# Kernel optimization log

Hardware: AMD Instinct MI355X
Metric: run time of the kernel (lower is better)

## Reference

```python
import jax, jax.numpy as jnp
import numpy as np

DIM = 768
NUM_HEADS = 12
HEAD_DIM = DIM // NUM_HEADS
SCALE = HEAD_DIM ** -0.5


def setup_inputs() -> dict:
    key = jax.random.key(0)
    ks = jax.random.split(key, 6)
    B, N, C = 4, 2048, DIM
    x = jax.random.normal(ks[0], (B, N, C), dtype=jnp.float32)
    qkv_weight = jax.random.normal(ks[1], (3 * C, C), dtype=jnp.float32) * (C ** -0.5)
    q_bias = jax.random.normal(ks[2], (C,), dtype=jnp.float32) * 0.02
    v_bias = jax.random.normal(ks[3], (C,), dtype=jnp.float32) * 0.02
    proj_weight = jax.random.normal(ks[4], (C, C), dtype=jnp.float32) * (C ** -0.5)
    proj_bias = jax.random.normal(ks[5], (C,), dtype=jnp.float32) * 0.02
    return {"x": x, "qkv_weight": qkv_weight, "q_bias": q_bias,
            "v_bias": v_bias, "proj_weight": proj_weight, "proj_bias": proj_bias}


def reference(x, qkv_weight, q_bias, v_bias, proj_weight, proj_bias):
    B, N, C = x.shape
    # bias = concat(q_bias, zeros_like(v_bias), v_bias)
    bias = jnp.concatenate([q_bias, jnp.zeros_like(v_bias), v_bias])
    qkv = x @ qkv_weight.T + bias                      # [B, N, 3C]
    qkv = qkv.reshape(B, N, 3, NUM_HEADS, HEAD_DIM)
    q, k, v = jnp.moveaxis(qkv, 2, 0)                  # each [B, N, H, hd]
    q = jnp.transpose(q, (0, 2, 1, 3)) * SCALE         # [B, H, N, hd]
    k = jnp.transpose(k, (0, 2, 1, 3))
    v = jnp.transpose(v, (0, 2, 1, 3))
    attn = jax.nn.softmax(jnp.einsum('bhqd,bhkd->bhqk', q, k), axis=-1)
    out = jnp.einsum('bhqk,bhkd->bhqd', attn, v)       # [B, H, N, hd]
    out = jnp.transpose(out, (0, 2, 1, 3)).reshape(B, N, C)
    return out @ proj_weight.T + proj_bias
```

## Files before the change

### kernel.cpp

```cpp
#include <hip/hip_runtime.h>
#include <cstdint>
#include <cstddef>

typedef _Float16 f16;
typedef _Float16 f16x8 __attribute__((ext_vector_type(8)));
typedef _Float16 f16x4 __attribute__((ext_vector_type(4)));
typedef __fp16 h16x2 __attribute__((ext_vector_type(2)));
typedef float f32x4 __attribute__((ext_vector_type(4)));
typedef float f32x16 __attribute__((ext_vector_type(16)));

#define DIM 768
#define NHEAD 12
#define HD 64
#define BATCH 4
#define SEQ 2048
#define MROWS (BATCH*SEQ)
#define C3 (3*DIM)
#define NBH (BATCH*NHEAD)

__device__ __forceinline__ f32x4 mfma32(f16x8 a, f16x8 b, f32x4 c) {
  return __builtin_amdgcn_mfma_f32_16x16x32_f16(a, b, c, 0, 0, 0);
}
__device__ __forceinline__ f32x16 mfma3232(f16x8 a, f16x8 b, f32x16 c) {
  return __builtin_amdgcn_mfma_f32_32x32x16_f16(a, b, c, 0, 0, 0);
}

__device__ __forceinline__ void gl2lds16(const void* g, void* l) {
  __builtin_amdgcn_global_load_lds(
      (const __attribute__((address_space(1))) void*)g,
      (__attribute__((address_space(3))) void*)l, 16, 0, 0);
}

__global__ __launch_bounds__(256) void k_convert(
    const float* __restrict__ x, const float* __restrict__ wqkv,
    const float* __restrict__ wproj,
    f16* __restrict__ xh, f16* __restrict__ wqh, f16* __restrict__ wph)
{
  const int NX = MROWS*DIM/4, NW = C3*DIM/4;
  int i = blockIdx.x * 256 + threadIdx.x;
  const float4* src; f16* dst; int idx;
  if (i < NX)         { src = (const float4*)x;     dst = xh;  idx = i; }
  else if (i < NX+NW) { src = (const float4*)wqkv;  dst = wqh; idx = i - NX; }
  else                { src = (const float4*)wproj; dst = wph; idx = i - NX - NW; }
  float4 v = src[idx];
  union { f16 h[4]; uint64_t u; } r;
  r.h[0] = (f16)v.x; r.h[1] = (f16)v.y; r.h[2] = (f16)v.z; r.h[3] = (f16)v.w;
  ((uint64_t*)dst)[idx] = r.u;
}

__device__ __forceinline__ void gemm_tile(
    const f16* __restrict__ A, const f16* __restrict__ B,
    int lda, int ldb, int K, int am0, int bn0,
    f16* smem, f32x4 acc[4][4])
{
  f16* sA0 = smem;         f16* sA1 = smem + 4096;
  f16* sB0 = smem + 8192;  f16* sB1 = smem + 12288;
  const int tid = threadIdx.x, wid = tid >> 6;
  const int lane = tid & 63, lane15 = lane & 15, quad = lane >> 4;
  const int wm = wid >> 1, wn = wid & 1;

  auto stage = [&](int k0, f16* sA, f16* sB) {
    #pragma unroll
    for (int i = 0; i < 2; i++) {
      int j = i*256 + tid;
      int row = j >> 2;
      int sc  = (j & 3) ^ ((row >> 1) & 3);
      gl2lds16(A + (size_t)(am0 + row)*lda + k0 + sc*8, sA + (i*256 + wid*64)*8);
      gl2lds16(B + (size_t)(bn0 + row)*ldb + k0 + sc*8, sB + (i*256 + wid*64)*8);
    }
  };

  const int NK = K >> 5;
  stage(0, sA0, sB0);
  for (int kk = 0; kk < NK; kk++) {
    f16* cA = (kk & 1) ? sA1 : sA0;
    f16* cB = (kk & 1) ? sB1 : sB0;
    __syncthreads();
    if (kk + 1 < NK)
      stage((kk + 1) << 5, (kk & 1) ? sA0 : sA1, (kk & 1) ? sB0 : sB1);
    f16x8 af[4], bf[4];
    #pragma unroll
    for (int t = 0; t < 4; t++) {
      int ra = wm*64 + t*16 + lane15;
      af[t] = *(const f16x8*)(cA + ra*32 + ((quad ^ ((ra >> 1) & 3)) << 3));
      int rb = wn*64 + t*16 + lane15;
      bf[t] = *(const f16x8*)(cB + rb*32 + ((quad ^ ((rb >> 1) & 3)) << 3));
    }
    #pragma unroll
    for (int mt = 0; mt < 4; mt++)
      #pragma unroll
      for (int nt = 0; nt < 4; nt++)
        acc[mt][nt] = mfma32(af[mt], bf[nt], acc[mt][nt]);
  }
}

__global__ __launch_bounds__(256, 4) void k_qkv(
    const f16* __restrict__ xh, const f16* __restrict__ wqh,
    const float* __restrict__ q_bias, const float* __restrict__ v_bias,
    f16* __restrict__ Qh, f16* __restrict__ Kh, f16* __restrict__ Vt)
{
  __shared__ f16 smem[16384];
  f32x4 acc[4][4];
  const f32x4 z4 = {0.f, 0.f, 0.f, 0.f};
  #pragma unroll
  for (int a = 0; a < 4; a++)
    #pragma unroll
    for (int b = 0; b < 4; b++) acc[a][b] = z4;

  const int tid = threadIdx.x, wid = tid >> 6, lane = tid & 63;
  const int lane15 = lane & 15, quad = lane >> 4;
  const int wm = wid >> 1, wn = wid & 1;
  const int cblk = blockIdx.x * 128;
  const int mblk = blockIdx.y * 128;
  const int bb = mblk >> 11, nbase = mblk & (SEQ - 1);
  const float QS = 0.125f * 1.4426950408889634f;

  if (cblk < 2*DIM) {
    gemm_tile(wqh, xh, DIM, DIM, DIM, cblk, mblk, smem, acc);
    const bool isQ = (cblk < DIM);
    #pragma unroll
    for (int mt = 0; mt < 4; mt++) {
      int c0 = cblk + wm*64 + mt*16 + quad*4;
      int cr = isQ ? c0 : (c0 - DIM);
      int h = cr >> 6, d0 = cr & 63;
      float4 qb4 = isQ ? *(const float4*)(q_bias + c0) : make_float4(0,0,0,0);
      f16* dst = isQ ? Qh : Kh;
      f16* base = dst + (((size_t)(bb*NHEAD + h)*SEQ + nbase) << 6) + d0;
      #pragma unroll
      for (int nt = 0; nt < 4; nt++) {
        int n = wn*64 + nt*16 + lane15;
        f32x4 v = acc[mt][nt];
        f16x4 hv;
        if (isQ) {
          hv[0] = (f16)((v[0] + qb4.x) * QS); hv[1] = (f16)((v[1] + qb4.y) * QS);
          hv[2] = (f16)((v[2] + qb4.z) * QS); hv[3] = (f16)((v[3] + qb4.w) * QS);
        } else {
          hv[0] = (f16)v[0]; hv[1] = (f16)v[1]; hv[2] = (f16)v[2]; hv[3] = (f16)v[3];
        }
        *(f16x4*)(base + ((size_t)n << 6)) = hv;
      }
    }
  } else {
    gemm_tile(xh, wqh, DIM, DIM, DIM, mblk, cblk, smem, acc);
    #pragma unroll
    for (int nt = 0; nt < 4; nt++) {
      int c = cblk + wn*64 + nt*16 + lane15;
      int c2 = c - 2*DIM;
      int h = c2 >> 6, d = c2 & 63;
      float b = v_bias[c2];
      f16* base = Vt + ((size_t)(bb*NHEAD + h)*HD + d)*SEQ + nbase;
      #pragma unroll
      for (int mt = 0; mt < 4; mt++) {
        int n0 = wm*64 + mt*16 + quad*4;
        f32x4 v = acc[mt][nt];
        f16x4 hv = {(f16)(v[0]+b), (f16)(v[1]+b), (f16)(v[2]+b), (f16)(v[3]+b)};
        *(f16x4*)(base + n0) = hv;
      }
    }
  }
}

#define KVT 128
#define NIT (SEQ/KVT)
__global__ __launch_bounds__(256, 3) void k_attn(
    const f16* __restrict__ Qh, const f16* __restrict__ Kh,
    const f16* __restrict__ Vt, f16* __restrict__ attnh)
{
  __shared__ f16 smem[2*8192 + 64*132];
  f16* sK0 = smem;
  f16* sK1 = smem + 8192;
  f16* sV  = smem + 16384;

  const int tid = threadIdx.x, wid = tid >> 6, lane = tid & 63;
  const int l31 = lane & 31, hi = lane >> 5;

  const int L = blockIdx.x;
  const int xcd = L & 7, kk = L >> 3;
  const int bh = xcd + 8*(kk >> 4);
  const int q0 = (kk & 15) * 128;
  const int qw = q0 + wid*32;

  const f16* Kbh = Kh + (size_t)bh*SEQ*HD;
  const f16* Vbh = Vt + (size_t)bh*HD*SEQ;

  f16x8 qf[4];
  #pragma unroll
  for (int ks = 0; ks < 4; ks++)
    qf[ks] = *(const f16x8*)(Qh + ((size_t)bh*SEQ + qw + l31)*HD + ks*16 + hi*8);

  const f32x16 z16 = {0.f,0.f,0.f,0.f, 0.f,0.f,0.f,0.f,
                      0.f,0.f,0.f,0.f, 0.f,0.f,0.f,0.f};
  f32x16 o0 = z16, o1 = z16, sacc = z16;
  f16x8 one8;
  #pragma unroll
  for (int j = 0; j < 8; j++) one8[j] = (f16)1.f;

  auto stageK = [&](int kv0, f16* sK) {
    #pragma unroll
    for (int i = 0; i < 4; i++) {
      int j = i*256 + tid;
      int row = j >> 3;
      int sc  = (j & 7) ^ (row & 7);
      gl2lds16(Kbh + (size_t)(kv0 + row)*HD + sc*8, sK + (i*256 + wid*64)*8);
    }
  };

  int koff[4];
  #pragma unroll
  for (int ks = 0; ks < 4; ks++)
    koff[ks] = l31*64 + (((2*ks + hi) ^ (l31 & 7)) << 3);

  const int vrow = tid >> 2, vcg = (tid & 3) * 32;
  const f16* vsrc = Vbh + (size_t)vrow*SEQ + vcg;

  stageK(0, sK0);
  f16x8 vreg[4];
  #pragma unroll
  for (int j = 0; j < 4; j++) vreg[j] = *(const f16x8*)(vsrc + j*8);

#define ASTEP(SCUR, SNXT, CC, HASNXT)                                         \
  do {                                                                        \
    const int vo = (CC)*32 + 4*hi;                                            \
    union { f16x4 q[2]; f16x8 v; } a00, a01, a10, a11;                        \
    a00.q[0] = *(const f16x4*)(sV + l31*132 + vo);                            \
    a00.q[1] = *(const f16x4*)(sV + l31*132 + vo + 8);                        \
    a01.q[0] = *(const f16x4*)(sV + l31*132 + vo + 16);                       \
    a01.q[1] = *(const f16x4*)(sV + l31*132 + vo + 24);                       \
    a10.q[0] = *(const f16x4*)(sV + (32 + l31)*132 + vo);                     \
    a10.q[1] = *(const f16x4*)(sV + (32 + l31)*132 + vo + 8);                 \
    a11.q[0] = *(const f16x4*)(sV + (32 + l31)*132 + vo + 16);                \
    a11.q[1] = *(const f16x4*)(sV + (32 + l31)*132 + vo + 24);                \
    unsigned hx[8];                                                           \
    _Pragma("unroll")                                                         \
    for (int r = 0; r < 8; r++) {                                             \
      union { h16x2 p2; unsigned u; } uu;                                     \
      uu.p2 = __builtin_amdgcn_cvt_pkrtz(                                     \
          __builtin_amdgcn_exp2f((SCUR)[2*r]),                                \
          __builtin_amdgcn_exp2f((SCUR)[2*r+1]));                             \
      hx[r] = uu.u;                                                           \
    }                                                                         \
    union { unsigned w[4]; f16x8 v; } b0u, b1u;                               \
    b0u.w[0]=hx[0]; b0u.w[1]=hx[1]; b0u.w[2]=hx[2]; b0u.w[3]=hx[3];           \
    b1u.w[0]=hx[4]; b1u.w[1]=hx[5]; b1u.w[2]=hx[6]; b1u.w[3]=hx[7];           \
    if (HASNXT) {                                                             \
      (SNXT) = z16;                                                           \
      __builtin_amdgcn_s_setprio(1);                                          \
      _Pragma("unroll")                                                       \
      for (int ks = 0; ks < 4; ks++) {                                        \
        f16x8 ka = *(const f16x8*)(cK + ((CC)+1)*2048 + koff[ks]);            \
        (SNXT) = mfma3232(ka, qf[ks], (SNXT));                                \
      }                                                                       \
      __builtin_amdgcn_s_setprio(0);                                          \
    }                                                                         \
    __builtin_amdgcn_s_setprio(1);                                            \
    sacc = mfma3232(one8, b0u.v, sacc);                                       \
    o0 = mfma3232(a00.v, b0u.v, o0);                                          \
    o1 = mfma3232(a10.v, b0u.v, o1);                                          \
    sacc = mfma3232(one8, b1u.v, sacc);                                       \
    o0 = mfma3232(a01.v, b1u.v, o0);                                          \
    o1 = mfma3232(a11.v, b1u.v, o1);                                          \
    __builtin_amdgcn_s_setprio(0);                                            \
  } while (0)

  for (int it = 0; it < NIT; it++) {
    f16* cK = (it & 1) ? sK1 : sK0;
    __syncthreads();
    #pragma unroll
    for (int j = 0; j < 4; j++) {
      union { f16x8 v; f16x4 h[2]; } u; u.v = vreg[j];
      *(f16x4*)(sV + vrow*132 + vcg + j*8)     = u.h[0];
      *(f16x4*)(sV + vrow*132 + vcg + j*8 + 4) = u.h[1];
    }
    __syncthreads();
    if (it + 1 < NIT) {
      stageK((it + 1)*KVT, (it & 1) ? sK0 : sK1);
      #pragma unroll
      for (int j = 0; j < 4; j++)
        vreg[j] = *(const f16x8*)(vsrc + (it + 1)*KVT + j*8);
    }

    f32x16 s0, s1;
    s0 = z16;
    __builtin_amdgcn_s_setprio(1);
    #pragma unroll
    for (int ks = 0; ks < 4; ks++) {
      f16x8 ka = *(const f16x8*)(cK + koff[ks]);
      s0 = mfma3232(ka, qf[ks], s0);
    }
    __builtin_amdgcn_s_setprio(0);
    ASTEP(s0, s1, 0, 1);
    ASTEP(s1, s0, 1, 1);
    ASTEP(s0, s1, 2, 1);
    ASTEP(s1, s0, 3, 0);
  }
#undef ASTEP

  const float inv = 1.f / sacc[0];

  __syncthreads();
  f16* tb = smem + wid * (32 * 72);
  #pragma unroll
  for (int g = 0; g < 4; g++) {
    f16x4 h0v = {(f16)(o0[4*g+0]*inv), (f16)(o0[4*g+1]*inv),
                 (f16)(o0[4*g+2]*inv), (f16)(o0[4*g+3]*inv)};
    *(f16x4*)(tb + l31*72 + g*8 + hi*4) = h0v;
    f16x4 h1v = {(f16)(o1[4*g+0]*inv), (f16)(o1[4*g+1]*inv),
                 (f16)(o1[4*g+2]*inv), (f16)(o1[4*g+3]*inv)};
    *(f16x4*)(tb + l31*72 + 32 + g*8 + hi*4) = h1v;
  }
  __syncthreads();
  const int b = bh / NHEAD, hh = bh % NHEAD;
  #pragma unroll
  for (int i = 0; i < 4; i++) {
    int row = i*8 + (lane >> 3);
    f16x8 rv = *(const f16x8*)(tb + row*72 + (lane & 7)*8);
    *(f16x8*)(attnh + ((size_t)b*SEQ + qw + row)*DIM + hh*HD + (lane & 7)*8) = rv;
  }
}

__global__ __launch_bounds__(256, 4) void k_proj(
    const f16* __restrict__ ah, const f16* __restrict__ wph,
    const float* __restrict__ pbias, float* __restrict__ out)
{
  __shared__ f16 smem[16384];
  f32x4 acc[4][4];
  const f32x4 z4 = {0.f, 0.f, 0.f, 0.f};
  #pragma unroll
  for (int a = 0; a < 4; a++)
    #pragma unroll
    for (int b = 0; b < 4; b++) acc[a][b] = z4;

  const int cblk = blockIdx.y * 128;
  const int mblk = blockIdx.x * 128;
  gemm_tile(wph, ah, DIM, DIM, DIM, cblk, mblk, smem, acc);

  const int tid = threadIdx.x, wid = tid >> 6, lane = tid & 63;
  const int lane15 = lane & 15, quad = lane >> 4;
  const int wm = wid >> 1, wn = wid & 1;
  #pragma unroll
  for (int mt = 0; mt < 4; mt++) {
    int c0 = cblk + wm*64 + mt*16 + quad*4;
    float4 b4 = *(const float4*)(pbias + c0);
    #pragma unroll
    for (int nt = 0; nt < 4; nt++) {
      int m = mblk + wn*64 + nt*16 + lane15;
      f32x4 v = acc[mt][nt];
      float4 r = make_float4(v[0]+b4.x, v[1]+b4.y, v[2]+b4.z, v[3]+b4.w);
      *(float4*)(out + (size_t)m*DIM + c0) = r;
    }
  }
}

extern "C" void kernel_launch(void* const* d_in, const int* in_sizes, int n_in,
                              void* d_out, int out_size, void* d_ws, size_t ws_size,
                              hipStream_t stream) {
  const float* x    = (const float*)d_in[0];
  const float* wqkv = (const float*)d_in[1];
  const float* qb   = (const float*)d_in[2];
  const float* vb   = (const float*)d_in[3];
  const float* wp   = (const float*)d_in[4];
  const float* pb   = (const float*)d_in[5];
  float* out = (float*)d_out;

  f16* p = (f16*)d_ws;
  f16* xh  = p; p += (size_t)MROWS*DIM;
  f16* wqh = p; p += (size_t)C3*DIM;
  f16* wph = p; p += (size_t)DIM*DIM;
  f16* Qh  = p; p += (size_t)NBH*SEQ*HD;
  f16* Kh  = p; p += (size_t)NBH*SEQ*HD;
  f16* Vt  = p; p += (size_t)NBH*SEQ*HD;
  f16* attnh = xh;

  k_convert<<<8448, 256, 0, stream>>>(x, wqkv, wp, xh, wqh, wph);
  k_qkv<<<dim3(C3/128, MROWS/128), 256, 0, stream>>>(xh, wqh, qb, vb, Qh, Kh, Vt);
  k_attn<<<dim3((SEQ/128)*NBH), 256, 0, stream>>>(Qh, Kh, Vt, attnh);
  k_proj<<<dim3(MROWS/128, DIM/128), 256, 0, stream>>>(attnh, wph, pb, out);
}
```

Measured before the change: 219.5 us.

## Swizzle GEMM block order per XCD and halve proj tile width

Both GEMM kernels now use a 1D grid whose block index is remapped so that blocks landing on the same XCD (round-robin by index mod 8) share the same activation row band, improving L2 reuse of the A/B tiles. The projection GEMM switches to a 64x128 tile with a new gemm_tile64 helper, doubling its block count from 384 to 768 to fill more CUs. The smaller proj tile lowers arithmetic intensity per block and re-reads activations more often.

```diff
diff --git a/kernel.cpp b/kernel.cpp
--- a/kernel.cpp
+++ b/kernel.cpp
@@ -94,6 +94,59 @@
   }
 }
 
+__device__ __forceinline__ void gemm_tile64(
+    const f16* __restrict__ A, const f16* __restrict__ B,
+    int lda, int ldb, int K, int am0, int bn0,
+    f16* smem, f32x4 acc[2][4])
+{
+  f16* sA0 = smem;         f16* sA1 = smem + 2048;
+  f16* sB0 = smem + 4096;  f16* sB1 = smem + 8192;
+  const int tid = threadIdx.x, wid = tid >> 6;
+  const int lane = tid & 63, lane15 = lane & 15, quad = lane >> 4;
+  const int wm = wid >> 1, wn = wid & 1;
+
+  auto stage = [&](int k0, f16* sA, f16* sB) {
+    {
+      int row = tid >> 2;
+      int sc  = (tid & 3) ^ ((row >> 1) & 3);
+      gl2lds16(A + (size_t)(am0 + row)*lda + k0 + sc*8, sA + (wid*64)*8);
+    }
+    #pragma unroll
+    for (int i = 0; i < 2; i++) {
+      int j = i*256 + tid;
+      int row = j >> 2;
+      int sc  = (j & 3) ^ ((row >> 1) & 3);
+      gl2lds16(B + (size_t)(bn0 + row)*ldb + k0 + sc*8, sB + (i*256 + wid*64)*8);
+    }
+  };
+
+  const int NK = K >> 5;
+  stage(0, sA0, sB0);
+  for (int kk = 0; kk < NK; kk++) {
+    f16* cA = (kk & 1) ? sA1 : sA0;
+    f16* cB = (kk & 1) ? sB1 : sB0;
+    __syncthreads();
+    if (kk + 1 < NK)
+      stage((kk + 1) << 5, (kk & 1) ? sA0 : sA1, (kk & 1) ? sB0 : sB1);
+    f16x8 af[2], bf[4];
+    #pragma unroll
+    for (int t = 0; t < 2; t++) {
+      int ra = wm*32 + t*16 + lane15;
+      af[t] = *(const f16x8*)(cA + ra*32 + ((quad ^ ((ra >> 1) & 3)) << 3));
+    }
+    #pragma unroll
+    for (int t = 0; t < 4; t++) {
+      int rb = wn*64 + t*16 + lane15;
+      bf[t] = *(const f16x8*)(cB + rb*32 + ((quad ^ ((rb >> 1) & 3)) << 3));
+    }
+    #pragma unroll
+    for (int mt = 0; mt < 2; mt++)
+      #pragma unroll
+      for (int nt = 0; nt < 4; nt++)
+        acc[mt][nt] = mfma32(af[mt], bf[nt], acc[mt][nt]);
+  }
+}
+
 __global__ __launch_bounds__(256, 4) void k_qkv(
     const f16* __restrict__ xh, const f16* __restrict__ wqh,
     const float* __restrict__ q_bias, const float* __restrict__ v_bias,
@@ -110,8 +163,10 @@
   const int tid = threadIdx.x, wid = tid >> 6, lane = tid & 63;
   const int lane15 = lane & 15, quad = lane >> 4;
   const int wm = wid >> 1, wn = wid & 1;
-  const int cblk = blockIdx.x * 128;
-  const int mblk = blockIdx.y * 128;
+  const int L = blockIdx.x;
+  const int xcd = L & 7, kk = L >> 3;
+  const int cblk = (kk % 18) * 128;
+  const int mblk = (xcd * 8 + kk / 18) * 128;
   const int bb = mblk >> 11, nbase = mblk & (SEQ - 1);
   const float QS = 0.125f * 1.4426950408889634f;
 
@@ -322,24 +377,26 @@
     const f16* __restrict__ ah, const f16* __restrict__ wph,
     const float* __restrict__ pbias, float* __restrict__ out)
 {
-  __shared__ f16 smem[16384];
-  f32x4 acc[4][4];
+  __shared__ f16 smem[12288];
+  f32x4 acc[2][4];
   const f32x4 z4 = {0.f, 0.f, 0.f, 0.f};
   #pragma unroll
-  for (int a = 0; a < 4; a++)
+  for (int a = 0; a < 2; a++)
     #pragma unroll
     for (int b = 0; b < 4; b++) acc[a][b] = z4;
 
-  const int cblk = blockIdx.y * 128;
-  const int mblk = blockIdx.x * 128;
-  gemm_tile(wph, ah, DIM, DIM, DIM, cblk, mblk, smem, acc);
+  const int L = blockIdx.x;
+  const int xcd = L & 7, kk = L >> 3;
+  const int cblk = (kk % 12) * 64;
+  const int mblk = (xcd * 8 + kk / 12) * 128;
+  gemm_tile64(wph, ah, DIM, DIM, DIM, cblk, mblk, smem, acc);
 
   const int tid = threadIdx.x, wid = tid >> 6, lane = tid & 63;
   const int lane15 = lane & 15, quad = lane >> 4;
   const int wm = wid >> 1, wn = wid & 1;
   #pragma unroll
-  for (int mt = 0; mt < 4; mt++) {
-    int c0 = cblk + wm*64 + mt*16 + quad*4;
+  for (int mt = 0; mt < 2; mt++) {
+    int c0 = cblk + wm*32 + mt*16 + quad*4;
     float4 b4 = *(const float4*)(pbias + c0);
     #pragma unroll
     for (int nt = 0; nt < 4; nt++) {
@@ -372,7 +429,7 @@
   f16* attnh = xh;
 
   k_convert<<<8448, 256, 0, stream>>>(x, wqkv, wp, xh, wqh, wph);
-  k_qkv<<<dim3(C3/128, MROWS/128), 256, 0, stream>>>(xh, wqh, qb, vb, Qh, Kh, Vt);
+  k_qkv<<<1152, 256, 0, stream>>>(xh, wqh, qb, vb, Qh, Kh, Vt);
   k_attn<<<dim3((SEQ/128)*NBH), 256, 0, stream>>>(Qh, Kh, Vt, attnh);
-  k_proj<<<dim3(MROWS/128, DIM/128), 256, 0, stream>>>(attnh, wph, pb, out);
-}
+  k_proj<<<768, 256, 0, stream>>>(attnh, wph, pb, out);
+}
```

Measured after the change: 227.4 us. 1.04x slower.
